# Kernel optimization log

Hardware: AMD Instinct MI355X
Metric: run time of the kernel (lower is better)

The kernel has to match this reference:

```python
import jax, jax.numpy as jnp
import numpy as np
from jax import lax

B, S, H, I, E, K = 4, 4096, 1024, 3584, 8, 2


def setup_inputs() -> dict:
    key = jax.random.key(0)
    ks = jax.random.split(key, 5)
    scale_h = 1.0 / np.sqrt(H)
    scale_i = 1.0 / np.sqrt(I)
    return {
        "hidden_states": jax.random.normal(ks[0], (B, S, H), dtype=jnp.float32),
        "gate_w": jax.random.normal(ks[1], (E, H), dtype=jnp.float32) * scale_h,
        "w1": jax.random.normal(ks[2], (E, H, I), dtype=jnp.float32) * scale_h,
        "w3": jax.random.normal(ks[3], (E, H, I), dtype=jnp.float32) * scale_h,
        "w2": jax.random.normal(ks[4], (E, I, H), dtype=jnp.float32) * scale_i,
        "top_k": K,
    }


def reference(hidden_states, gate_w, w1, w3, w2, top_k):
    b, s, h = hidden_states.shape
    n_experts = gate_w.shape[0]
    x = hidden_states.reshape(-1, h)  # [T, H]

    # Router: softmax in fp32, top-k, renormalize (Mixtral style)
    logits = x @ gate_w.T  # [T, E]
    probs = jax.nn.softmax(logits.astype(jnp.float32), axis=-1)
    top_w, top_idx = lax.top_k(probs, top_k)  # [T, K]
    top_w = top_w.astype(x.dtype)
    top_w = top_w / jnp.sum(top_w, axis=-1, keepdims=True)

    # Per-token, per-expert combine weight: [T, E]
    one_hot = jax.nn.one_hot(top_idx, n_experts, dtype=x.dtype)  # [T, K, E]
    w_full = jnp.einsum("tk,tke->te", top_w, one_hot)

    out = jnp.zeros_like(x)
    for e in range(n_experts):  # fixed small loop over experts
        hidden = jax.nn.silu(x @ w1[e]) * (x @ w3[e])  # SwiGLU, [T, I]
        y = hidden @ w2[e]  # [T, H]
        out = out + y * w_full[:, e:e + 1]
    return out.reshape(b, s, h)
```

## Files before the change

kernel.cpp:

```cpp
#include <hip/hip_runtime.h>
#include <hip/hip_bf16.h>

#define T_TOK 16384
#define H_DIM 1024
#define I_DIM 3584
#define E_NUM 8
#define N13   7168
#define TOTP  32768

typedef __attribute__((ext_vector_type(8))) short s16x8;
typedef __attribute__((ext_vector_type(4))) float f32x4;
typedef unsigned short u16;

__device__ __forceinline__ u16 f2bf(float f) {
    union { float f; unsigned u; } c; c.f = f;
    unsigned r = c.u + 0x7fffu + ((c.u >> 16) & 1u);
    return (u16)(r >> 16);
}

__device__ __forceinline__ void glds16(const u16* g, u16* l) {
    __builtin_amdgcn_global_load_lds(
        (const __attribute__((address_space(1))) unsigned int*)g,
        (__attribute__((address_space(3))) unsigned int*)l,
        16, 0, 0);
}

__global__ __launch_bounds__(64)
void router_k(const float* __restrict__ x, const float* __restrict__ gw,
              int* __restrict__ tk_idx, float* __restrict__ tk_w,
              int* __restrict__ counts, u16* __restrict__ xb)
{
    int t = blockIdx.x;
    int lane = threadIdx.x;
    const float* xr = x + (size_t)t * H_DIM;
    float xv[16];
#pragma unroll
    for (int j = 0; j < 16; j++) xv[j] = xr[j * 64 + lane];
    u16* xo = xb + (size_t)t * H_DIM;
#pragma unroll
    for (int j = 0; j < 16; j++) xo[j * 64 + lane] = f2bf(xv[j]);
    float lg[E_NUM];
#pragma unroll
    for (int e = 0; e < E_NUM; e++) {
        const float* g = gw + e * H_DIM;
        float s = 0.f;
#pragma unroll
        for (int j = 0; j < 16; j++) s += xv[j] * g[j * 64 + lane];
#pragma unroll
        for (int off = 32; off > 0; off >>= 1) s += __shfl_xor(s, off, 64);
        lg[e] = s;
    }
    if (lane == 0) {
        int i1 = 0; float m1 = lg[0];
#pragma unroll
        for (int e = 1; e < E_NUM; e++) if (lg[e] > m1) { m1 = lg[e]; i1 = e; }
        int i2 = -1; float m2 = -3.4e38f;
#pragma unroll
        for (int e = 0; e < E_NUM; e++) if (e != i1 && lg[e] > m2) { m2 = lg[e]; i2 = e; }
        float p1 = 1.f / (1.f + __expf(m2 - m1));
        float p2 = 1.f - p1;
        tk_idx[t * 2]     = i1;
        tk_idx[t * 2 + 1] = i2;
        tk_w[t * 2]       = p1;
        tk_w[t * 2 + 1]   = p2;
        atomicAdd(&counts[i1], 1);
        atomicAdd(&counts[i2], 1);
    }
}

__global__ void offsets_k(const int* __restrict__ counts, int* __restrict__ offsets,
                          int* __restrict__ cursor)
{
    if (threadIdx.x == 0 && blockIdx.x == 0) {
        int acc = 0;
        for (int e = 0; e < E_NUM; e++) { offsets[e] = acc; cursor[e] = acc; acc += counts[e]; }
        offsets[E_NUM] = acc;
    }
}

__global__ __launch_bounds__(256)
void scatter_k(const int* __restrict__ tk_idx, const float* __restrict__ tk_w,
               int* __restrict__ cursor, int* __restrict__ perm, float* __restrict__ pw,
               int* __restrict__ posmap)
{
    int t = blockIdx.x * 256 + threadIdx.x;
    if (t >= T_TOK) return;
#pragma unroll
    for (int k = 0; k < 2; k++) {
        int e = tk_idx[t * 2 + k];
        int pos = atomicAdd(&cursor[e], 1);
        perm[pos] = t;
        pw[pos]   = tk_w[t * 2 + k];
        posmap[t * 2 + k] = pos;
    }
}

__global__ __launch_bounds__(256)
void tcvtw_k(const float* __restrict__ src, u16* __restrict__ dst,
             int M, int N, int mat, int dmul)
{
    size_t eo_s = (size_t)blockIdx.z * M * N;
    size_t eo_d = (size_t)blockIdx.z * (size_t)M * N * dmul;
    __shared__ u16 tl[32][136];
    int t = threadIdx.x;
    int m0 = blockIdx.y * 128, n0 = blockIdx.x * 32;
    int lr = t >> 3, lc = (t & 7) * 4;
#pragma unroll
    for (int it = 0; it < 4; it++) {
        int mr = it * 32 + lr;
        float4 v = *reinterpret_cast<const float4*>(src + eo_s + (size_t)(m0 + mr) * N + n0 + lc);
        tl[lc + 0][mr] = f2bf(v.x); tl[lc + 1][mr] = f2bf(v.y);
        tl[lc + 2][mr] = f2bf(v.z); tl[lc + 3][mr] = f2bf(v.w);
    }
    __syncthreads();
    int sn = t >> 4, sm = (t & 15) * 8;
#pragma unroll
    for (int it = 0; it < 2; it++) {
        int nr = it * 16 + sn;
        int ic = n0 + nr;
        int orow = (mat < 0) ? ic : (((ic >> 4) << 5) + (mat << 4) + (ic & 15));
        s16x8 v = *reinterpret_cast<const s16x8*>(&tl[nr][sm]);
        *reinterpret_cast<s16x8*>(dst + eo_d + (size_t)orow * M + m0 + sm) = v;
    }
}


__global__ __launch_bounds__(512, 2)
void gemm1_k(const u16* __restrict__ xb, const u16* __restrict__ w13t,
             const int* __restrict__ offsets, const int* __restrict__ perm,
             const float* __restrict__ pw, u16* __restrict__ hidden)
{
    int e = blockIdx.z;
    int base = offsets[e];
    int cnt  = offsets[e + 1] - base;
    int m0 = blockIdx.y * 256;
    if (m0 >= cnt) return;
    int n0 = blockIdx.x * 256;

    __shared__ u16 As[2][256 * 64];
    __shared__ u16 Bs[2][256 * 64];

    int t = threadIdx.x;
    int lane = t & 63, wave = t >> 6;
    int wm = (wave >> 2) * 128;
    int wn = (wave & 3) * 64;
    int l15 = lane & 15, quad = lane >> 4;
    int x7 = l15 & 7;
    int s0 = (quad ^ x7) * 8;
    int s1 = ((4 + quad) ^ x7) * 8;

    int sr = t >> 3;
    int ss = t & 7;
    const u16* aptr[4];
    const u16* bptr[4];
#pragma unroll
    for (int l = 0; l < 4; l++) {
        int ra = l * 64 + sr;
        int pr = m0 + ra; if (pr > cnt - 1) pr = cnt - 1;
        aptr[l] = xb + (size_t)perm[base + pr] * H_DIM + (ss ^ (ra & 7)) * 8;
        bptr[l] = w13t + (size_t)e * N13 * H_DIM + (size_t)(n0 + ra) * H_DIM + (ss ^ (ra & 7)) * 8;
    }

    auto STAGE = [&](int buf, int k0) {
#pragma unroll
        for (int l = 0; l < 4; l++) glds16(aptr[l] + k0, &As[buf][l * 4096 + t * 8]);
#pragma unroll
        for (int l = 0; l < 4; l++) glds16(bptr[l] + k0, &Bs[buf][l * 4096 + t * 8]);
    };

    f32x4 acc[8][4] = {};
    const int NT = H_DIM / 64;

    STAGE(0, 0);
    for (int kt = 0; kt < NT; ++kt) {
        int cur = kt & 1;
        if (kt + 1 < NT) {
            STAGE(cur ^ 1, (kt + 1) * 64);
            asm volatile("s_waitcnt vmcnt(8)" ::: "memory");
        } else {
            asm volatile("s_waitcnt vmcnt(0)" ::: "memory");
        }
        __builtin_amdgcn_s_barrier();
        asm volatile("" ::: "memory");
        const u16* Ab = As[cur];
        const u16* Bb = Bs[cur];
        s16x8 af[8][2];
#pragma unroll
        for (int i2 = 0; i2 < 8; i2++) {
            int row = wm + i2 * 16 + l15;
            af[i2][0] = *reinterpret_cast<const s16x8*>(Ab + row * 64 + s0);
            af[i2][1] = *reinterpret_cast<const s16x8*>(Ab + row * 64 + s1);
        }
#pragma unroll
        for (int nh = 0; nh < 2; nh++) {
            s16x8 bf[2][2];
#pragma unroll
            for (int j = 0; j < 2; j++) {
                int row = wn + nh * 32 + j * 16 + l15;
                bf[j][0] = *reinterpret_cast<const s16x8*>(Bb + row * 64 + s0);
                bf[j][1] = *reinterpret_cast<const s16x8*>(Bb + row * 64 + s1);
            }
            __builtin_amdgcn_s_setprio(1);
#pragma unroll
            for (int kk = 0; kk < 2; kk++)
#pragma unroll
            for (int j = 0; j < 2; j++)
#pragma unroll
            for (int i2 = 0; i2 < 8; i2++)
                acc[i2][nh * 2 + j] = __builtin_amdgcn_mfma_f32_16x16x32_bf16(
                    af[i2][kk], bf[j][kk], acc[i2][nh * 2 + j], 0, 0, 0);
            __builtin_amdgcn_s_setprio(0);
        }
        __builtin_amdgcn_s_barrier();
        asm volatile("" ::: "memory");
    }

    int hc0 = (n0 + wn) >> 1;
#pragma unroll
    for (int i = 0; i < 8; i++) {
        int rowoff = (i >> 2) * 64 + (i & 3) * 16 + quad * 4;
#pragma unroll
        for (int r = 0; r < 4; r++) {
            int p = m0 + wm + rowoff + r;
            if (p < cnt) {
                float w = pw[base + p];
                u16* hrow = hidden + (size_t)(base + p) * I_DIM + hc0;
#pragma unroll
                for (int nh = 0; nh < 2; nh++) {
                    float z1 = acc[i][nh * 2 + 0][r];
                    float z3 = acc[i][nh * 2 + 1][r];
                    float hv = (z1 / (1.f + __expf(-z1))) * z3 * w;
                    hrow[nh * 16 + l15] = f2bf(hv);
                }
            }
        }
    }
}

__global__ __launch_bounds__(512, 2)
void gemm2_k(const u16* __restrict__ hidden, const u16* __restrict__ w2t,
             const int* __restrict__ offsets, float* __restrict__ ybuf)
{
    int e = blockIdx.z;
    int base = offsets[e];
    int cnt  = offsets[e + 1] - base;
    int m0 = blockIdx.y * 256;
    if (m0 >= cnt) return;
    int n0 = blockIdx.x * 256;

    __shared__ u16 As[2][256 * 64];
    __shared__ u16 Bs[2][256 * 64];

    int t = threadIdx.x;
    int lane = t & 63, wave = t >> 6;
    int wm = (wave >> 2) * 128;
    int wn = (wave & 3) * 64;
    int l15 = lane & 15, quad = lane >> 4;
    int x7 = l15 & 7;
    int s0 = (quad ^ x7) * 8;
    int s1 = ((4 + quad) ^ x7) * 8;

    int sr = t >> 3;
    int ss = t & 7;
    const u16* aptr[4];
    const u16* bptr[4];
    const u16* wb = w2t + (size_t)e * H_DIM * I_DIM;
#pragma unroll
    for (int l = 0; l < 4; l++) {
        int ra = l * 64 + sr;
        int pr = m0 + ra; if (pr > cnt - 1) pr = cnt - 1;
        aptr[l] = hidden + (size_t)(base + pr) * I_DIM + (ss ^ (ra & 7)) * 8;
        bptr[l] = wb + (size_t)(n0 + ra) * I_DIM + (ss ^ (ra & 7)) * 8;
    }

    auto STAGE = [&](int buf, int k0) {
#pragma unroll
        for (int l = 0; l < 4; l++) glds16(aptr[l] + k0, &As[buf][l * 4096 + t * 8]);
#pragma unroll
        for (int l = 0; l < 4; l++) glds16(bptr[l] + k0, &Bs[buf][l * 4096 + t * 8]);
    };

    f32x4 acc[8][4] = {};
    const int NT = I_DIM / 64;

    STAGE(0, 0);
    for (int kt = 0; kt < NT; ++kt) {
        int cur = kt & 1;
        if (kt + 1 < NT) {
            STAGE(cur ^ 1, (kt + 1) * 64);
            asm volatile("s_waitcnt vmcnt(8)" ::: "memory");
        } else {
            asm volatile("s_waitcnt vmcnt(0)" ::: "memory");
        }
        __builtin_amdgcn_s_barrier();
        asm volatile("" ::: "memory");
        const u16* Ab = As[cur];
        const u16* Bb = Bs[cur];
        s16x8 af[8][2];
#pragma unroll
        for (int i2 = 0; i2 < 8; i2++) {
            int row = wm + i2 * 16 + l15;
            af[i2][0] = *reinterpret_cast<const s16x8*>(Ab + row * 64 + s0);
            af[i2][1] = *reinterpret_cast<const s16x8*>(Ab + row * 64 + s1);
        }
#pragma unroll
        for (int nh = 0; nh < 2; nh++) {
            s16x8 bf[2][2];
#pragma unroll
            for (int j = 0; j < 2; j++) {
                int row = wn + nh * 32 + j * 16 + l15;
                bf[j][0] = *reinterpret_cast<const s16x8*>(Bb + row * 64 + s0);
                bf[j][1] = *reinterpret_cast<const s16x8*>(Bb + row * 64 + s1);
            }
            __builtin_amdgcn_s_setprio(1);
#pragma unroll
            for (int kk = 0; kk < 2; kk++)
#pragma unroll
            for (int j = 0; j < 2; j++)
#pragma unroll
            for (int i2 = 0; i2 < 8; i2++)
                acc[i2][nh * 2 + j] = __builtin_amdgcn_mfma_f32_16x16x32_bf16(
                    af[i2][kk], bf[j][kk], acc[i2][nh * 2 + j], 0, 0, 0);
            __builtin_amdgcn_s_setprio(0);
        }
        __builtin_amdgcn_s_barrier();
        asm volatile("" ::: "memory");
    }

#pragma unroll
    for (int i = 0; i < 8; i++) {
        int rowoff = (i >> 2) * 64 + (i & 3) * 16 + quad * 4;
#pragma unroll
        for (int r = 0; r < 4; r++) {
            int p = m0 + wm + rowoff + r;
            if (p < cnt) {
                float* orow = ybuf + (size_t)(base + p) * H_DIM + n0 + wn;
#pragma unroll
                for (int nh = 0; nh < 2; nh++)
#pragma unroll
                for (int j = 0; j < 2; j++)
                    orow[nh * 32 + j * 16 + l15] = acc[i][nh * 2 + j][r];
            }
        }
    }
}

__global__ __launch_bounds__(256)
void combine_k(const float* __restrict__ ybuf, const int* __restrict__ posmap,
               float* __restrict__ out)
{
    int t = blockIdx.x;
    int c = threadIdx.x * 4;
    int pa = posmap[t * 2];
    int pb = posmap[t * 2 + 1];
    float4 a = *reinterpret_cast<const float4*>(ybuf + (size_t)pa * H_DIM + c);
    float4 b = *reinterpret_cast<const float4*>(ybuf + (size_t)pb * H_DIM + c);
    float4 o = make_float4(a.x + b.x, a.y + b.y, a.z + b.z, a.w + b.w);
    *reinterpret_cast<float4*>(out + (size_t)t * H_DIM + c) = o;
}

extern "C" void kernel_launch(void* const* d_in, const int* in_sizes, int n_in,
                              void* d_out, int out_size, void* d_ws, size_t ws_size,
                              hipStream_t stream)
{
    (void)in_sizes; (void)n_in; (void)ws_size; (void)out_size;
    const float* x  = (const float*)d_in[0];
    const float* gw = (const float*)d_in[1];
    const float* w1 = (const float*)d_in[2];
    const float* w3 = (const float*)d_in[3];
    const float* w2 = (const float*)d_in[4];
    float* out = (float*)d_out;

    char* ws = (char*)d_ws;
    int*   counts  = (int*)ws;
    int*   offsets = counts + 8;
    int*   cursor  = offsets + 9;
    int*   tk_idx  = (int*)(ws + 128);
    float* tk_w    = (float*)(ws + 128 + 131072);
    int*   perm    = (int*)(ws + 128 + 2 * 131072);
    float* pw      = (float*)(ws + 128 + 3 * 131072);
    int*   posmap  = (int*)(ws + 128 + 4 * 131072);
    u16* xb     = (u16*)(ws + (1 << 20));
    u16* w13t   = xb + 16777216ull;
    u16* w2t    = w13t + 58720256ull;
    u16* hidden = w2t + 29360128ull;
    float* ybuf = (float*)(ws + (1 << 20));

    hipMemsetAsync(ws, 0, 128, stream);
    router_k<<<T_TOK, 64, 0, stream>>>(x, gw, tk_idx, tk_w, counts, xb);
    offsets_k<<<1, 64, 0, stream>>>(counts, offsets, cursor);
    scatter_k<<<T_TOK / 256, 256, 0, stream>>>(tk_idx, tk_w, cursor, perm, pw, posmap);
    tcvtw_k<<<dim3(I_DIM / 32, H_DIM / 128, E_NUM), 256, 0, stream>>>(w1, w13t, H_DIM, I_DIM, 0, 2);
    tcvtw_k<<<dim3(I_DIM / 32, H_DIM / 128, E_NUM), 256, 0, stream>>>(w3, w13t, H_DIM, I_DIM, 1, 2);
    tcvtw_k<<<dim3(H_DIM / 32, I_DIM / 128, E_NUM), 256, 0, stream>>>(w2, w2t, I_DIM, H_DIM, -1, 1);
    gemm1_k<<<dim3(N13 / 256, 64, E_NUM), 512, 0, stream>>>(xb, w13t, offsets, perm, pw, hidden);
    gemm2_k<<<dim3(H_DIM / 256, 64, E_NUM), 512, 0, stream>>>(hidden, w2t, offsets, ybuf);
    combine_k<<<T_TOK, 256, 0, stream>>>(ybuf, posmap, out);
}
```

Before: 1.895 ms.

## Restructure MoE GEMM main loops into fine-grained interleaved load/compute pipeline

Both expert GEMM kernels replace the simple double-buffered K loop with an 8-phase schedule per two K tiles. Each phase issues a slice of global-to-LDS loads, reads a subset of A/B fragments from LDS, and runs 16 MFMAs, with barriers and lgkm/vm waits between phases. The aim is to spread memory traffic across compute phases, keep the matrix units fed, and cut the long stall at the per-tile barrier. It adds many more barriers, and its correctness depends on the exact vmcnt accounting and on buffer reuse ordering.

```diff
diff --git a/kernel.cpp b/kernel.cpp
--- a/kernel.cpp
+++ b/kernel.cpp
@@ -11,6 +11,11 @@
 typedef __attribute__((ext_vector_type(8))) short s16x8;
 typedef __attribute__((ext_vector_type(4))) float f32x4;
 typedef unsigned short u16;
+
+#define BAR()    asm volatile("s_barrier" ::: "memory")
+#define WAITL()  asm volatile("s_waitcnt lgkmcnt(0)" ::: "memory")
+#define WAITV4() asm volatile("s_waitcnt vmcnt(4)" ::: "memory")
+#define WAITV0() asm volatile("s_waitcnt vmcnt(0)" ::: "memory")
 
 __device__ __forceinline__ u16 f2bf(float f) {
     union { float f; unsigned u; } c; c.f = f;
@@ -137,8 +142,8 @@
     if (m0 >= cnt) return;
     int n0 = blockIdx.x * 256;
 
-    __shared__ u16 As[2][256 * 64];
-    __shared__ u16 Bs[2][256 * 64];
+    __shared__ u16 As[2][16384];
+    __shared__ u16 Bs[2][16384];
 
     int t = threadIdx.x;
     int lane = t & 63, wave = t >> 6;
@@ -146,8 +151,8 @@
     int wn = (wave & 3) * 64;
     int l15 = lane & 15, quad = lane >> 4;
     int x7 = l15 & 7;
-    int s0 = (quad ^ x7) * 8;
-    int s1 = ((4 + quad) ^ x7) * 8;
+    int sl0 = (quad ^ x7) * 8;
+    int sl1 = ((4 + quad) ^ x7) * 8;
 
     int sr = t >> 3;
     int ss = t & 7;
@@ -161,59 +166,71 @@
         bptr[l] = w13t + (size_t)e * N13 * H_DIM + (size_t)(n0 + ra) * H_DIM + (ss ^ (ra & 7)) * 8;
     }
 
-    auto STAGE = [&](int buf, int k0) {
-#pragma unroll
-        for (int l = 0; l < 4; l++) glds16(aptr[l] + k0, &As[buf][l * 4096 + t * 8]);
-#pragma unroll
-        for (int l = 0; l < 4; l++) glds16(bptr[l] + k0, &Bs[buf][l * 4096 + t * 8]);
-    };
-
-    f32x4 acc[8][4] = {};
-    const int NT = H_DIM / 64;
-
-    STAGE(0, 0);
-    for (int kt = 0; kt < NT; ++kt) {
-        int cur = kt & 1;
-        if (kt + 1 < NT) {
-            STAGE(cur ^ 1, (kt + 1) * 64);
-            asm volatile("s_waitcnt vmcnt(8)" ::: "memory");
-        } else {
-            asm volatile("s_waitcnt vmcnt(0)" ::: "memory");
-        }
-        __builtin_amdgcn_s_barrier();
-        asm volatile("" ::: "memory");
-        const u16* Ab = As[cur];
-        const u16* Bb = Bs[cur];
-        s16x8 af[8][2];
+    u16* A0l = &As[0][0]; u16* A1l = &As[1][0];
+    u16* B0l = &Bs[0][0]; u16* B1l = &Bs[1][0];
+
+    auto STG = [&](u16* lbase, const u16* const* gptr, int h, int koff) {
+        glds16(gptr[2 * h]     + koff, lbase + (2 * h)     * 4096 + t * 8);
+        glds16(gptr[2 * h + 1] + koff, lbase + (2 * h + 1) * 4096 + t * 8);
+    };
+    auto RDA = [&](const u16* Ab, s16x8* af, int kksel) {
 #pragma unroll
         for (int i2 = 0; i2 < 8; i2++) {
             int row = wm + i2 * 16 + l15;
-            af[i2][0] = *reinterpret_cast<const s16x8*>(Ab + row * 64 + s0);
-            af[i2][1] = *reinterpret_cast<const s16x8*>(Ab + row * 64 + s1);
-        }
-#pragma unroll
-        for (int nh = 0; nh < 2; nh++) {
-            s16x8 bf[2][2];
-#pragma unroll
-            for (int j = 0; j < 2; j++) {
-                int row = wn + nh * 32 + j * 16 + l15;
-                bf[j][0] = *reinterpret_cast<const s16x8*>(Bb + row * 64 + s0);
-                bf[j][1] = *reinterpret_cast<const s16x8*>(Bb + row * 64 + s1);
-            }
-            __builtin_amdgcn_s_setprio(1);
-#pragma unroll
-            for (int kk = 0; kk < 2; kk++)
-#pragma unroll
-            for (int j = 0; j < 2; j++)
-#pragma unroll
-            for (int i2 = 0; i2 < 8; i2++)
-                acc[i2][nh * 2 + j] = __builtin_amdgcn_mfma_f32_16x16x32_bf16(
-                    af[i2][kk], bf[j][kk], acc[i2][nh * 2 + j], 0, 0, 0);
-            __builtin_amdgcn_s_setprio(0);
-        }
-        __builtin_amdgcn_s_barrier();
-        asm volatile("" ::: "memory");
-    }
+            af[i2] = *reinterpret_cast<const s16x8*>(Ab + row * 64 + (kksel ? sl1 : sl0));
+        }
+    };
+    auto RDB = [&](const u16* Bb, s16x8* bf, int nh, int kksel) {
+#pragma unroll
+        for (int j = 0; j < 2; j++) {
+            int row = wn + nh * 32 + j * 16 + l15;
+            bf[j] = *reinterpret_cast<const s16x8*>(Bb + row * 64 + (kksel ? sl1 : sl0));
+        }
+    };
+
+    f32x4 acc[8][4] = {};
+    auto MF = [&](const s16x8* af, const s16x8* bf, int nh) {
+        __builtin_amdgcn_s_setprio(1);
+#pragma unroll
+        for (int j = 0; j < 2; j++)
+#pragma unroll
+        for (int i2 = 0; i2 < 8; i2++)
+            acc[i2][nh * 2 + j] = __builtin_amdgcn_mfma_f32_16x16x32_bf16(
+                af[i2], bf[j], acc[i2][nh * 2 + j], 0, 0, 0);
+        __builtin_amdgcn_s_setprio(0);
+    };
+
+    const int NT = H_DIM / 64;
+    const int NTI = NT / 2;
+
+    STG(A0l, aptr, 0, 0);  STG(A0l, aptr, 1, 0);
+    STG(B0l, bptr, 0, 0);  STG(B0l, bptr, 1, 0);
+    STG(A1l, aptr, 0, 64); STG(A1l, aptr, 1, 64);
+    WAITV4(); BAR();
+
+    for (int it = 0; it < NTI; ++it) {
+        int ko1 = (2 * it + 1) * 64;
+        int ko2 = (2 * it + 2 < NT) ? (2 * it + 2) * 64 : 0;
+        int ko3 = (2 * it + 3 < NT) ? (2 * it + 3) * 64 : 0;
+        s16x8 af0[8], af1[8], bfa[2], bfb[2];
+        RDA(A0l, af0, 0); RDB(B0l, bfa, 0, 0); STG(B1l, bptr, 0, ko1);
+        BAR(); WAITL(); MF(af0, bfa, 0); BAR();
+        RDA(A0l, af1, 1); RDB(B0l, bfb, 0, 1); STG(B1l, bptr, 1, ko1);
+        BAR(); WAITL(); MF(af1, bfb, 0); BAR();
+        RDB(B0l, bfa, 1, 0); STG(A0l, aptr, 0, ko2);
+        BAR(); WAITL(); MF(af0, bfa, 1); BAR();
+        RDB(B0l, bfb, 1, 1); STG(A0l, aptr, 1, ko2);
+        BAR(); WAITL(); MF(af1, bfb, 1); WAITV4(); BAR();
+        RDA(A1l, af0, 0); RDB(B1l, bfa, 0, 0); STG(B0l, bptr, 0, ko2);
+        BAR(); WAITL(); MF(af0, bfa, 0); BAR();
+        RDA(A1l, af1, 1); RDB(B1l, bfb, 0, 1); STG(B0l, bptr, 1, ko2);
+        BAR(); WAITL(); MF(af1, bfb, 0); BAR();
+        RDB(B1l, bfa, 1, 0); STG(A1l, aptr, 0, ko3);
+        BAR(); WAITL(); MF(af0, bfa, 1); BAR();
+        RDB(B1l, bfb, 1, 1); STG(A1l, aptr, 1, ko3);
+        BAR(); WAITL(); MF(af1, bfb, 1); WAITV4(); BAR();
+    }
+    WAITV0();
 
     int hc0 = (n0 + wn) >> 1;
 #pragma unroll
@@ -248,8 +265,8 @@
     if (m0 >= cnt) return;
     int n0 = blockIdx.x * 256;
 
-    __shared__ u16 As[2][256 * 64];
-    __shared__ u16 Bs[2][256 * 64];
+    __shared__ u16 As[2][16384];
+    __shared__ u16 Bs[2][16384];
 
     int t = threadIdx.x;
     int lane = t & 63, wave = t >> 6;
@@ -257,8 +274,8 @@
     int wn = (wave & 3) * 64;
     int l15 = lane & 15, quad = lane >> 4;
     int x7 = l15 & 7;
-    int s0 = (quad ^ x7) * 8;
-    int s1 = ((4 + quad) ^ x7) * 8;
+    int sl0 = (quad ^ x7) * 8;
+    int sl1 = ((4 + quad) ^ x7) * 8;
 
     int sr = t >> 3;
     int ss = t & 7;
@@ -273,59 +290,71 @@
         bptr[l] = wb + (size_t)(n0 + ra) * I_DIM + (ss ^ (ra & 7)) * 8;
     }
 
-    auto STAGE = [&](int buf, int k0) {
-#pragma unroll
-        for (int l = 0; l < 4; l++) glds16(aptr[l] + k0, &As[buf][l * 4096 + t * 8]);
-#pragma unroll
-        for (int l = 0; l < 4; l++) glds16(bptr[l] + k0, &Bs[buf][l * 4096 + t * 8]);
-    };
-
-    f32x4 acc[8][4] = {};
-    const int NT = I_DIM / 64;
-
-    STAGE(0, 0);
-    for (int kt = 0; kt < NT; ++kt) {
-        int cur = kt & 1;
-        if (kt + 1 < NT) {
-            STAGE(cur ^ 1, (kt + 1) * 64);
-            asm volatile("s_waitcnt vmcnt(8)" ::: "memory");
-        } else {
-            asm volatile("s_waitcnt vmcnt(0)" ::: "memory");
-        }
-        __builtin_amdgcn_s_barrier();
-        asm volatile("" ::: "memory");
-        const u16* Ab = As[cur];
-        const u16* Bb = Bs[cur];
-        s16x8 af[8][2];
+    u16* A0l = &As[0][0]; u16* A1l = &As[1][0];
+    u16* B0l = &Bs[0][0]; u16* B1l = &Bs[1][0];
+
+    auto STG = [&](u16* lbase, const u16* const* gptr, int h, int koff) {
+        glds16(gptr[2 * h]     + koff, lbase + (2 * h)     * 4096 + t * 8);
+        glds16(gptr[2 * h + 1] + koff, lbase + (2 * h + 1) * 4096 + t * 8);
+    };
+    auto RDA = [&](const u16* Ab, s16x8* af, int kksel) {
 #pragma unroll
         for (int i2 = 0; i2 < 8; i2++) {
             int row = wm + i2 * 16 + l15;
-            af[i2][0] = *reinterpret_cast<const s16x8*>(Ab + row * 64 + s0);
-            af[i2][1] = *reinterpret_cast<const s16x8*>(Ab + row * 64 + s1);
-        }
-#pragma unroll
-        for (int nh = 0; nh < 2; nh++) {
-            s16x8 bf[2][2];
-#pragma unroll
-            for (int j = 0; j < 2; j++) {
-                int row = wn + nh * 32 + j * 16 + l15;
-                bf[j][0] = *reinterpret_cast<const s16x8*>(Bb + row * 64 + s0);
-                bf[j][1] = *reinterpret_cast<const s16x8*>(Bb + row * 64 + s1);
-            }
-            __builtin_amdgcn_s_setprio(1);
-#pragma unroll
-            for (int kk = 0; kk < 2; kk++)
-#pragma unroll
-            for (int j = 0; j < 2; j++)
-#pragma unroll
-            for (int i2 = 0; i2 < 8; i2++)
-                acc[i2][nh * 2 + j] = __builtin_amdgcn_mfma_f32_16x16x32_bf16(
-                    af[i2][kk], bf[j][kk], acc[i2][nh * 2 + j], 0, 0, 0);
-            __builtin_amdgcn_s_setprio(0);
-        }
-        __builtin_amdgcn_s_barrier();
-        asm volatile("" ::: "memory");
-    }
+            af[i2] = *reinterpret_cast<const s16x8*>(Ab + row * 64 + (kksel ? sl1 : sl0));
+        }
+    };
+    auto RDB = [&](const u16* Bb, s16x8* bf, int nh, int kksel) {
+#pragma unroll
+        for (int j = 0; j < 2; j++) {
+            int row = wn + nh * 32 + j * 16 + l15;
+            bf[j] = *reinterpret_cast<const s16x8*>(Bb + row * 64 + (kksel ? sl1 : sl0));
+        }
+    };
+
+    f32x4 acc[8][4] = {};
+    auto MF = [&](const s16x8* af, const s16x8* bf, int nh) {
+        __builtin_amdgcn_s_setprio(1);
+#pragma unroll
+        for (int j = 0; j < 2; j++)
+#pragma unroll
+        for (int i2 = 0; i2 < 8; i2++)
+            acc[i2][nh * 2 + j] = __builtin_amdgcn_mfma_f32_16x16x32_bf16(
+                af[i2], bf[j], acc[i2][nh * 2 + j], 0, 0, 0);
+        __builtin_amdgcn_s_setprio(0);
+    };
+
+    const int NT = I_DIM / 64;
+    const int NTI = NT / 2;
+
+    STG(A0l, aptr, 0, 0);  STG(A0l, aptr, 1, 0);
+    STG(B0l, bptr, 0, 0);  STG(B0l, bptr, 1, 0);
+    STG(A1l, aptr, 0, 64); STG(A1l, aptr, 1, 64);
+    WAITV4(); BAR();
+
+    for (int it = 0; it < NTI; ++it) {
+        int ko1 = (2 * it + 1) * 64;
+        int ko2 = (2 * it + 2 < NT) ? (2 * it + 2) * 64 : 0;
+        int ko3 = (2 * it + 3 < NT) ? (2 * it + 3) * 64 : 0;
+        s16x8 af0[8], af1[8], bfa[2], bfb[2];
+        RDA(A0l, af0, 0); RDB(B0l, bfa, 0, 0); STG(B1l, bptr, 0, ko1);
+        BAR(); WAITL(); MF(af0, bfa, 0); BAR();
+        RDA(A0l, af1, 1); RDB(B0l, bfb, 0, 1); STG(B1l, bptr, 1, ko1);
+        BAR(); WAITL(); MF(af1, bfb, 0); BAR();
+        RDB(B0l, bfa, 1, 0); STG(A0l, aptr, 0, ko2);
+        BAR(); WAITL(); MF(af0, bfa, 1); BAR();
+        RDB(B0l, bfb, 1, 1); STG(A0l, aptr, 1, ko2);
+        BAR(); WAITL(); MF(af1, bfb, 1); WAITV4(); BAR();
+        RDA(A1l, af0, 0); RDB(B1l, bfa, 0, 0); STG(B0l, bptr, 0, ko2);
+        BAR(); WAITL(); MF(af0, bfa, 0); BAR();
+        RDA(A1l, af1, 1); RDB(B1l, bfb, 0, 1); STG(B0l, bptr, 1, ko2);
+        BAR(); WAITL(); MF(af1, bfb, 0); BAR();
+        RDB(B1l, bfa, 1, 0); STG(A1l, aptr, 0, ko3);
+        BAR(); WAITL(); MF(af0, bfa, 1); BAR();
+        RDB(B1l, bfb, 1, 1); STG(A1l, aptr, 1, ko3);
+        BAR(); WAITL(); MF(af1, bfb, 1); WAITV4(); BAR();
+    }
+    WAITV0();
 
 #pragma unroll
     for (int i = 0; i < 8; i++) {
```

Result: faster. 1.795 ms (-5.3%).
